# Kernel tuning notes

Measured on AMD Instinct MI355X. Metric: run time of the kernel, lower is better.

## Reference

```python
import jax, jax.numpy as jnp
import numpy as np

TEMP_DIM = 36      # V
HIDDEN   = 128     # d
HEADS    = 4
STATIC   = 16
MAX_LEN  = 500
SEQ_T    = 256
BATCH    = 32


def _xavier(k, shape):
    lim = np.sqrt(6.0 / (shape[0] + shape[1]))
    return jax.random.uniform(k, shape, jnp.float32, -lim, lim)


def setup_inputs() -> dict:
    d, V, S, T, B = HIDDEN, TEMP_DIM, STATIC, SEQ_T, BATCH
    key = jax.random.key(0)
    ks = jax.random.split(key, 16)
    return dict(
        Xtemp=jax.random.normal(ks[0], (T, B, V), jnp.float32),
        Xtimes=jax.random.uniform(ks[1], (T, B, 1), jnp.float32) * MAX_LEN,
        Xstatic=jax.random.normal(ks[2], (B, S), jnp.float32),
        mask=jax.random.randint(ks[3], (T, B, V), 0, 2, jnp.int32),
        # MultiHeadAttention params
        Wq=_xavier(ks[4], (d, d)), Wk=_xavier(ks[5], (d, d)), Wv=_xavier(ks[6], (d, d)),
        # grouped Conv1d(V, V*d, 1, groups=V): per-variable scale+bias -> (V,d)
        temp_w=jax.random.normal(ks[7], (V, d), jnp.float32) * 0.5,
        temp_b=jnp.zeros((V, d), jnp.float32),
        # static embedding Linear(S, V*d)
        emb_W=_xavier(ks[8], (S, V * d)), emb_b=jnp.zeros((V * d,), jnp.float32),
        # MLP: Conv1d(V*d,4d,1)+BN+GELU, Conv1d(4d,d,1)+BN+GELU
        mlp_W1=_xavier(ks[9], (4 * d, V * d)), mlp_b1=jnp.zeros((4 * d,), jnp.float32),
        bn1_g=jnp.ones((4 * d,), jnp.float32), bn1_b=jnp.zeros((4 * d,), jnp.float32),
        mlp_W2=_xavier(ks[10], (d, 4 * d)), mlp_b2=jnp.zeros((d,), jnp.float32),
        bn2_g=jnp.ones((d,), jnp.float32), bn2_b=jnp.zeros((d,), jnp.float32),
        ln_g=jnp.ones((d,), jnp.float32), ln_b=jnp.zeros((d,), jnp.float32),
    )


def _batchnorm(x, g, b):
    # train-mode BatchNorm1d over (B, T) for x:(B, C, T), biased variance, eps=1e-5
    mu = x.mean((0, 2), keepdims=True)
    var = x.var((0, 2), keepdims=True)
    return (x - mu) * jax.lax.rsqrt(var + 1e-5) * g[None, :, None] + b[None, :, None]


def reference(Xtemp, Xtimes, Xstatic, mask, Wq, Wk, Wv, temp_w, temp_b,
              emb_W, emb_b, mlp_W1, mlp_b1, bn1_g, bn1_b,
              mlp_W2, mlp_b2, bn2_g, bn2_b, ln_g, ln_b):
    T, B, V = Xtemp.shape
    d = Wq.shape[0]
    h = HEADS
    dk = d // h

    xt = Xtemp.transpose(1, 2, 0)                      # (B,V,T)
    m = mask.astype(jnp.float32).transpose(1, 2, 0)    # (B,V,T)

    # grouped 1x1 conv == per-variable affine lift to d channels
    Htemp = xt[:, :, None, :] * temp_w[None, :, :, None] + temp_b[None, :, :, None]  # (B,V,d,T)
    Htemp = Htemp.transpose(0, 2, 1, 3)                # (B,d,V,T)

    # positional encoding
    timescales = jnp.power(jnp.float32(MAX_LEN), jnp.linspace(0.0, 1.0, d // 2))
    scaled = Xtimes / timescales                       # (T,B,d//2)
    pe = jnp.concatenate([jnp.sin(scaled), jnp.cos(scaled)], axis=-1)  # (T,B,d)
    Hpos = pe.transpose(1, 2, 0)[:, :, None, :]        # (B,d,1,T)

    emb = (Xstatic @ emb_W + emb_b).reshape(B, V, d).transpose(0, 2, 1)[..., None]  # (B,d,V,1)
    H = Htemp + Hpos + emb                             # (B,d,V,T)

    # masked temporal mean per variable
    mk = m[:, None]                                    # (B,1,V,T)
    h2 = (H * mk).sum(-1)                              # (B,d,V)
    lt = mk.sum(-1) + 1.0                              # (B,1,V)
    h4 = (h2 / lt).transpose(0, 2, 1)                  # (B,V,d)

    # multi-head variable-vs-variable scores
    scale = 1.0 / np.sqrt(dk).astype(np.float32)
    q = (h4 @ Wq).reshape(B, V, h, dk) * scale
    k = (h4 @ Wk).reshape(B, V, h, dk) * scale
    A = jnp.einsum('bvhd,buhd->bhvu', q, k)            # (B,h,V,V)
    mean_v = h4 @ Wv                                   # (B,V,d)

    # per-timestep key masking, broadcast softmax over last (key-variable) dim
    key_mask = m.transpose(0, 2, 1)                    # (B,T,V)
    A4 = A[:, :, None, :, :] - 1e6 * (1.0 - key_mask[:, None, :, None, :])  # (B,h,T,V,V)
    S = jax.nn.softmax(A4, axis=-1)                    # (B,h,T,V,V)

    H2 = H.reshape(B, h, dk, V, T)
    v2 = jnp.einsum('bhtvu,bhdut->bhdvt', S, H2)       # (B,h,dk,V,T)
    v3 = v2.reshape(B, d, V, T)
    v4 = v3 + mean_v.transpose(0, 2, 1)[:, :, :, None]
    v5 = v4.reshape(B, d * V, T)

    y1 = jnp.einsum('bct,oc->bot', v5, mlp_W1) + mlp_b1[None, :, None]
    y1 = jax.nn.gelu(_batchnorm(y1, bn1_g, bn1_b), approximate=False)
    y2 = jnp.einsum('bct,oc->bot', y1, mlp_W2) + mlp_b2[None, :, None]
    z = jax.nn.gelu(_batchnorm(y2, bn2_g, bn2_b), approximate=False)   # (B,d,T)

    # residual LayerNorm over channel dim
    zt = z.transpose(0, 2, 1)                          # (B,T,d)
    mu = zt.mean(-1, keepdims=True)
    var = zt.var(-1, keepdims=True)
    zn = (zt - mu) * jax.lax.rsqrt(var + 1e-5) * ln_g + ln_b
    return z + zn.transpose(0, 2, 1)                   # (B,d,T)
```

## Files before the change

### kernel.cpp

```cpp
#include <hip/hip_runtime.h>
#include <hip/hip_bf16.h>
#include <math.h>

#define T_  256
#define B_  32
#define V_  36
#define D_  128
#define H_  4
#define DK_ 32
#define S_  16
#define D4_ 512
#define K1_ 4608
#define M_  8192

typedef __hip_bfloat16 bf16;
typedef __attribute__((ext_vector_type(8))) short short8;
typedef __attribute__((ext_vector_type(4))) float f32x4;

__device__ __forceinline__ float gelu_f(float x){
    return 0.5f * x * (1.0f + erff(x * 0.70710678118654752f));
}

__device__ __forceinline__ float dot4(float4 a, float4 b){
    return fmaf(a.x, b.x, fmaf(a.y, b.y, fmaf(a.z, b.z, a.w * b.w)));
}

__device__ __forceinline__ unsigned short bf16_bits(float x){
    bf16 h = __float2bfloat16(x);
    return *reinterpret_cast<unsigned short*>(&h);
}

#define GLD16(g, l) __builtin_amdgcn_global_load_lds( \
    (const __attribute__((address_space(1))) void*)(g), \
    (__attribute__((address_space(3))) void*)(l), 16, 0, 0)

__global__ void k_pe(const float* __restrict__ Xtimes, const float* __restrict__ Xtemp,
                     const int* __restrict__ mask, float* __restrict__ PE,
                     float* __restrict__ QQ){
    int bt = blockIdx.x;
    int b = bt >> 8, t = bt & 255;
    int tid = threadIdx.x;
    float x = Xtimes[t*B_ + b];
    int i = (tid < 64) ? tid : tid - 64;
    float sc = x * exp2f(-(float)i * (8.965784284662087f / 63.0f));
    PE[(size_t)bt*D_ + tid] = (tid < 64) ? sinf(sc) : cosf(sc);
    if(tid < 64){
        float m = 0.f, xv = 0.f;
        if(tid < V_){
            m  = (float)mask[(t*B_ + b)*V_ + tid];
            xv = Xtemp[(t*B_ + b)*V_ + tid];
        }
        float s = m;
        #pragma unroll
        for(int off = 32; off > 0; off >>= 1) s += __shfl_xor(s, off);
        if(tid < V_){
            float q0 = (s > 0.f) ? m : 1.f;
            float q1 = (s > 0.f) ? m*xv : xv;
            QQ[(size_t)bt*80 + tid]      = q1;
            QQ[(size_t)bt*80 + 40 + tid] = q0;
        }
    }
}

__global__ void k_cb(const float* __restrict__ Xstatic, const float* __restrict__ embW,
                     const float* __restrict__ embB, const float* __restrict__ tempB,
                     float* __restrict__ CB, float* __restrict__ cbP){
    int bv = blockIdx.x;
    int b = bv / V_, v = bv - (bv / V_) * V_;
    int dd = threadIdx.x;
    int c = v*D_ + dd;
    float acc = tempB[c] + embB[c];
    #pragma unroll
    for(int s = 0; s < S_; ++s) acc = fmaf(Xstatic[b*S_+s], embW[s*K1_ + c], acc);
    CB[(size_t)bv*D_ + dd] = acc;
    cbP[(((size_t)b*9 + (v >> 2))*D_ + dd)*4 + (v & 3)] = acc;
}

__global__ void k_packtw(const float* __restrict__ tempW, float* __restrict__ twP){
    int v = blockIdx.x, dd = threadIdx.x;
    twP[(((v >> 2))*D_ + dd)*4 + (v & 3)] = tempW[v*D_ + dd];
}

__global__ void k_h4(const float* __restrict__ Xtemp, const int* __restrict__ mask,
                     const float* __restrict__ PE, const float* __restrict__ tempW,
                     const float* __restrict__ CB, float* __restrict__ H4){
    __shared__ float s_m[T_];
    __shared__ float s_r0[256];
    __shared__ float s_r1[256];
    __shared__ float s_p[2][D_];
    int bv = blockIdx.x;
    int b = bv / V_, v = bv - (bv / V_) * V_;
    int tid = threadIdx.x;
    float mval = (float)mask[(tid*B_ + b)*V_ + v];
    float xval = Xtemp[(tid*B_ + b)*V_ + v];
    s_m[tid]  = mval;
    s_r0[tid] = mval;
    s_r1[tid] = mval * xval;
    __syncthreads();
    for(int off = 128; off > 0; off >>= 1){
        if(tid < off){ s_r0[tid] += s_r0[tid+off]; s_r1[tid] += s_r1[tid+off]; }
        __syncthreads();
    }
    float sm = s_r0[0], sx = s_r1[0];
    int dd = tid & 127, half = tid >> 7;
    float sp = 0.f;
    for(int tt = half*128; tt < half*128 + 128; ++tt)
        sp = fmaf(s_m[tt], PE[(size_t)(b*T_ + tt)*D_ + dd], sp);
    s_p[half][dd] = sp;
    __syncthreads();
    if(tid < D_){
        float spv = s_p[0][tid] + s_p[1][tid];
        float h2 = fmaf(sx, tempW[v*D_ + tid], fmaf(sm, CB[(size_t)bv*D_ + tid], spv));
        H4[(size_t)bv*D_ + tid] = h2 / (sm + 1.0f);
    }
}

__global__ void k_qkv(const float* __restrict__ H4, const float* __restrict__ Wq,
                      const float* __restrict__ Wk, const float* __restrict__ Wv,
                      float* __restrict__ QS, float* __restrict__ KS, float* __restrict__ MV){
    __shared__ float s_h[D_];
    int bv = blockIdx.x;
    int o = threadIdx.x;
    s_h[o] = H4[(size_t)bv*D_ + o];
    __syncthreads();
    float aq = 0.f, ak = 0.f, av = 0.f;
    #pragma unroll 8
    for(int kk = 0; kk < D_; ++kk){
        float hv = s_h[kk];
        aq = fmaf(hv, Wq[kk*D_ + o], aq);
        ak = fmaf(hv, Wk[kk*D_ + o], ak);
        av = fmaf(hv, Wv[kk*D_ + o], av);
    }
    const float scale = 0.17677669529663687f;
    QS[(size_t)bv*D_ + o] = aq * scale;
    KS[(size_t)bv*D_ + o] = ak * scale;
    MV[(size_t)bv*D_ + o] = av;
}

__global__ void k_attE(const float* __restrict__ QS, const float* __restrict__ KS,
                       float* __restrict__ E){
    int id = blockIdx.x;
    int v  = id % V_;
    int bh = id / V_;
    int hh = bh & 3, b = bh >> 2;
    int u = threadIdx.x;
    __shared__ float s_q[DK_];
    if(u < DK_) s_q[u] = QS[(size_t)(b*V_ + v)*D_ + hh*DK_ + u];
    __syncthreads();
    float a = -INFINITY;
    if(u < V_){
        a = 0.f;
        const float* kp = &KS[(size_t)(b*V_ + u)*D_ + hh*DK_];
        #pragma unroll
        for(int kk = 0; kk < DK_; ++kk) a = fmaf(s_q[kk], kp[kk], a);
    }
    float m = a;
    for(int off = 32; off > 0; off >>= 1) m = fmaxf(m, __shfl_xor(m, off));
    if(u < V_) E[(size_t)id*40 + u] = expf(a - m);
}

__global__ __launch_bounds__(256) void k_v5(const float* __restrict__ QQ,
        const float* __restrict__ Eg, const float* __restrict__ twP,
        const float* __restrict__ cbP, const float* __restrict__ MV,
        const float* __restrict__ PE, bf16* __restrict__ V5){
    __shared__ float s_E[4*1300];
    int bt = blockIdx.x;
    int b = bt >> 8;
    int tid = threadIdx.x;
    int vq = tid >> 6, hh = (tid >> 4) & 3, j = tid & 15;
    int dd0 = hh*32 + j, dd1 = dd0 + 16;

    for(int i = tid; i < 144*9; i += 256){
        int hv = i / 9, u4 = i - hv*9;
        int hq = hv / 36, vr = hv - hq*36;
        float4 e = *(const float4*)&Eg[((size_t)b*144 + hv)*40 + u4*4];
        *(float4*)&s_E[hq*1300 + (u4*36 + vr)*4] = e;
    }
    __syncthreads();

    float acc0[9] = {}, acc1[9] = {}, den[9] = {};
    const float* qq = &QQ[(size_t)bt*80];
    #pragma unroll 1
    for(int u4 = 0; u4 < 9; ++u4){
        float4 q1 = *(const float4*)&qq[u4*4];
        float4 q0 = *(const float4*)&qq[40 + u4*4];
        float4 tw0 = *(const float4*)&twP[(u4*D_ + dd0)*4];
        float4 tw1 = *(const float4*)&twP[(u4*D_ + dd1)*4];
        float4 cb0 = *(const float4*)&cbP[(((size_t)b*9 + u4)*D_ + dd0)*4];
        float4 cb1 = *(const float4*)&cbP[(((size_t)b*9 + u4)*D_ + dd1)*4];
        float4 w0, w1;
        w0.x = fmaf(q1.x, tw0.x, q0.x*cb0.x); w0.y = fmaf(q1.y, tw0.y, q0.y*cb0.y);
        w0.z = fmaf(q1.z, tw0.z, q0.z*cb0.z); w0.w = fmaf(q1.w, tw0.w, q0.w*cb0.w);
        w1.x = fmaf(q1.x, tw1.x, q0.x*cb1.x); w1.y = fmaf(q1.y, tw1.y, q0.y*cb1.y);
        w1.z = fmaf(q1.z, tw1.z, q0.z*cb1.z); w1.w = fmaf(q1.w, tw1.w, q0.w*cb1.w);
        const float* eb = &s_E[hh*1300 + (u4*36 + vq*9)*4];
        #pragma unroll
        for(int vv = 0; vv < 9; ++vv){
            float4 e = *(const float4*)&eb[vv*4];
            den[vv]  += dot4(e, q0);
            acc0[vv] += dot4(e, w0);
            acc1[vv] += dot4(e, w1);
        }
    }
    float pe0 = PE[(size_t)bt*D_ + dd0];
    float pe1 = PE[(size_t)bt*D_ + dd1];
    bf16* op0 = V5 + (size_t)bt*K1_ + dd0*V_ + vq*9;
    bf16* op1 = V5 + (size_t)bt*K1_ + dd1*V_ + vq*9;
    #pragma unroll
    for(int vv = 0; vv < 9; ++vv){
        float rd = 1.0f / den[vv];
        float m0v = MV[((size_t)b*V_ + vq*9 + vv)*D_ + dd0];
        float m1v = MV[((size_t)b*V_ + vq*9 + vv)*D_ + dd1];
        op0[vv] = __float2bfloat16(fmaf(acc0[vv], rd, m0v + pe0));
        op1[vv] = __float2bfloat16(fmaf(acc1[vv], rd, m1v + pe1));
    }
}

__global__ void k_cast(const float* __restrict__ src, bf16* __restrict__ dst){
    int i = (blockIdx.x*256 + threadIdx.x)*4;
    float4 v = *(const float4*)&src[i];
    dst[i+0] = __float2bfloat16(v.x);
    dst[i+1] = __float2bfloat16(v.y);
    dst[i+2] = __float2bfloat16(v.z);
    dst[i+3] = __float2bfloat16(v.w);
}

__global__ __launch_bounds__(256) void k_gemm1(const bf16* __restrict__ A,
        const bf16* __restrict__ Bw, const float* __restrict__ bias,
        float* __restrict__ C){
    __shared__ __align__(16) bf16 As[128*64];
    __shared__ __align__(16) bf16 Bs[64*64];
    int bid = blockIdx.x;
    int L = (bid & 7)*64 + (bid >> 3);
    int nb = L & 7, mb = L >> 3;
    int m0 = mb * 128, n0 = nb * 64;
    int tid = threadIdx.x;
    int w = tid >> 6, l = tid & 63;
    int wr = w >> 1, wc = w & 1;
    int r = l & 15, kg = l >> 4;
    f32x4 acc[4][2] = {};

    int sA0 = 0*256 + w*64 + l;
    int sA1 = 1*256 + w*64 + l;
    int sA2 = 2*256 + w*64 + l;
    int sA3 = 3*256 + w*64 + l;
    int sB0 = 0*256 + w*64 + l;
    int sB1 = 1*256 + w*64 + l;
    const bf16* gA0 = A + (size_t)(m0 + (sA0>>3))*K1_ + ((sA0&7) ^ ((sA0>>3)&7))*8;
    const bf16* gA1 = A + (size_t)(m0 + (sA1>>3))*K1_ + ((sA1&7) ^ ((sA1>>3)&7))*8;
    const bf16* gA2 = A + (size_t)(m0 + (sA2>>3))*K1_ + ((sA2&7) ^ ((sA2>>3)&7))*8;
    const bf16* gA3 = A + (size_t)(m0 + (sA3>>3))*K1_ + ((sA3&7) ^ ((sA3>>3)&7))*8;
    const bf16* gB0 = Bw + (size_t)(n0 + (sB0>>3))*K1_ + ((sB0&7) ^ ((sB0>>3)&7))*8;
    const bf16* gB1 = Bw + (size_t)(n0 + (sB1>>3))*K1_ + ((sB1&7) ^ ((sB1>>3)&7))*8;
    bf16* lA0 = &As[(0*256 + w*64)*8];
    bf16* lA1 = &As[(1*256 + w*64)*8];
    bf16* lA2 = &As[(2*256 + w*64)*8];
    bf16* lA3 = &As[(3*256 + w*64)*8];
    bf16* lB0 = &Bs[(0*256 + w*64)*8];
    bf16* lB1 = &Bs[(1*256 + w*64)*8];

    for(int k0 = 0; k0 < K1_; k0 += 64){
        GLD16(gA0 + k0, lA0);
        GLD16(gA1 + k0, lA1);
        GLD16(gA2 + k0, lA2);
        GLD16(gA3 + k0, lA3);
        GLD16(gB0 + k0, lB0);
        GLD16(gB1 + k0, lB1);
        __syncthreads();
        short8 af[2][4], bfr[2][2];
        #pragma unroll
        for(int kh = 0; kh < 2; ++kh){
            #pragma unroll
            for(int m = 0; m < 4; ++m){
                int row = wr*64 + m*16 + r;
                int e = (row*64 + kh*32 + kg*8) ^ ((r & 7) << 3);
                af[kh][m] = *(const short8*)&As[e];
            }
            #pragma unroll
            for(int n = 0; n < 2; ++n){
                int row = wc*32 + n*16 + r;
                int e = (row*64 + kh*32 + kg*8) ^ ((r & 7) << 3);
                bfr[kh][n] = *(const short8*)&Bs[e];
            }
        }
        #pragma unroll
        for(int kh = 0; kh < 2; ++kh)
            #pragma unroll
            for(int m = 0; m < 4; ++m)
                #pragma unroll
                for(int n = 0; n < 2; ++n)
                    acc[m][n] = __builtin_amdgcn_mfma_f32_16x16x32_bf16(
                                    af[kh][m], bfr[kh][n], acc[m][n], 0, 0, 0);
        __syncthreads();
    }
    #pragma unroll
    for(int m = 0; m < 4; ++m){
        int rowb = m0 + wr*64 + m*16 + kg*4;
        #pragma unroll
        for(int n = 0; n < 2; ++n){
            int col = n0 + wc*32 + n*16 + r;
            float bv = bias[col];
            #pragma unroll
            for(int i = 0; i < 4; ++i)
                C[(size_t)(rowb + i)*D4_ + col] = acc[m][n][i] + bv;
        }
    }
}

__global__ void k_stats(const float* __restrict__ X, int C, float* __restrict__ ST){
    int r0 = blockIdx.x * 32;
    int tid = threadIdx.x;
    for(int c = tid; c < C; c += 256){
        float s = 0.f, q = 0.f;
        for(int r = 0; r < 32; ++r){
            float v = X[(size_t)(r0 + r)*C + c];
            s += v;
            q = fmaf(v, v, q);
        }
        atomicAdd(&ST[c], s);
        atomicAdd(&ST[C + c], q);
    }
}

__global__ void k_bnfin(const float* __restrict__ ST, const float* __restrict__ g,
                        const float* __restrict__ bb, int C, float* __restrict__ P){
    int c = blockIdx.x * blockDim.x + threadIdx.x;
    if(c < C){
        float mu  = ST[c] * (1.0f / M_);
        float var = ST[C + c] * (1.0f / M_) - mu*mu;
        float sc  = g[c] * rsqrtf(var + 1e-5f);
        P[c]     = sc;
        P[C + c] = bb[c] - mu*sc;
    }
}

__global__ __launch_bounds__(256) void k_gemm2(const float* __restrict__ Y1,
        const float* __restrict__ P1, const bf16* __restrict__ W2b,
        const float* __restrict__ b2, float* __restrict__ Z){
    __shared__ __align__(16) bf16 As[64*64];
    __shared__ __align__(16) bf16 Bs[64*64];
    int m0 = blockIdx.x * 64, n0 = blockIdx.y * 64;
    int tid = threadIdx.x;
    int w = tid >> 6, l = tid & 63;
    int wr = w >> 1, wc = w & 1;
    int r = l & 15, kg = l >> 4;
    f32x4 acc[2][2] = {};

    int sB0 = 0*256 + w*64 + l;
    int sB1 = 1*256 + w*64 + l;
    const bf16* gB0 = W2b + (size_t)(n0 + (sB0>>3))*D4_ + ((sB0&7) ^ ((sB0>>3)&7))*8;
    const bf16* gB1 = W2b + (size_t)(n0 + (sB1>>3))*D4_ + ((sB1&7) ^ ((sB1>>3)&7))*8;
    bf16* lB0 = &Bs[(0*256 + w*64)*8];
    bf16* lB1 = &Bs[(1*256 + w*64)*8];

    int arow = tid >> 2;
    int akq  = (tid & 3) * 16;
    int k8a  = (tid & 3) * 2;
    int e0 = arow*64 + ((k8a+0) ^ (arow & 7))*8;
    int e1 = arow*64 + ((k8a+1) ^ (arow & 7))*8;

    for(int k0 = 0; k0 < D4_; k0 += 64){
        GLD16(gB0 + k0, lB0);
        GLD16(gB1 + k0, lB1);
        const float* ya = &Y1[(size_t)(m0 + arow)*D4_ + k0 + akq];
        const float* sc = &P1[k0 + akq];
        const float* sh = &P1[D4_ + k0 + akq];
        unsigned int pk[8];
        #pragma unroll
        for(int q = 0; q < 4; ++q){
            float4 y  = *(const float4*)&ya[q*4];
            float4 s4 = *(const float4*)&sc[q*4];
            float4 h4 = *(const float4*)&sh[q*4];
            float a0 = gelu_f(fmaf(y.x, s4.x, h4.x));
            float a1 = gelu_f(fmaf(y.y, s4.y, h4.y));
            float a2 = gelu_f(fmaf(y.z, s4.z, h4.z));
            float a3 = gelu_f(fmaf(y.w, s4.w, h4.w));
            pk[q*2+0] = (unsigned)bf16_bits(a0) | ((unsigned)bf16_bits(a1) << 16);
            pk[q*2+1] = (unsigned)bf16_bits(a2) | ((unsigned)bf16_bits(a3) << 16);
        }
        uint4 wA0 = {pk[0], pk[1], pk[2], pk[3]};
        uint4 wA1 = {pk[4], pk[5], pk[6], pk[7]};
        *(uint4*)&As[e0] = wA0;
        *(uint4*)&As[e1] = wA1;
        __syncthreads();
        short8 af[2][2], bfr[2][2];
        #pragma unroll
        for(int kh = 0; kh < 2; ++kh){
            #pragma unroll
            for(int m = 0; m < 2; ++m){
                int row = wr*32 + m*16 + r;
                int e = (row*64 + kh*32 + kg*8) ^ ((r & 7) << 3);
                af[kh][m] = *(const short8*)&As[e];
            }
            #pragma unroll
            for(int n = 0; n < 2; ++n){
                int row = wc*32 + n*16 + r;
                int e = (row*64 + kh*32 + kg*8) ^ ((r & 7) << 3);
                bfr[kh][n] = *(const short8*)&Bs[e];
            }
        }
        #pragma unroll
        for(int kh = 0; kh < 2; ++kh)
            #pragma unroll
            for(int m = 0; m < 2; ++m)
                #pragma unroll
                for(int n = 0; n < 2; ++n)
                    acc[m][n] = __builtin_amdgcn_mfma_f32_16x16x32_bf16(
                                    af[kh][m], bfr[kh][n], acc[m][n], 0, 0, 0);
        __syncthreads();
    }
    #pragma unroll
    for(int m = 0; m < 2; ++m){
        int rowb = m0 + wr*32 + m*16 + kg*4;
        #pragma unroll
        for(int n = 0; n < 2; ++n){
            int col = n0 + wc*32 + n*16 + r;
            float bv = b2[col];
            #pragma unroll
            for(int i = 0; i < 4; ++i)
                Z[(size_t)(rowb + i)*D_ + col] = acc[m][n][i] + bv;
        }
    }
}

__global__ __launch_bounds__(256) void k_final(const float* __restrict__ Z,
        const float* __restrict__ P2, const float* __restrict__ lng,
        const float* __restrict__ lnb, float* __restrict__ out){
    __shared__ float s_z[64*129];
    __shared__ float s_mu[64];
    __shared__ float s_rs[64];
    int b  = blockIdx.x >> 2;
    int t0 = (blockIdx.x & 3) * 64;
    int tid = threadIdx.x;
    #pragma unroll
    for(int i = 0; i < 32; ++i){
        int idx = tid + i*256;
        int row = idx >> 7, col = idx & 127;
        float v = Z[(size_t)(b*T_ + t0 + row)*D_ + col];
        s_z[row*129 + col] = gelu_f(fmaf(v, P2[col], P2[D_ + col]));
    }
    __syncthreads();
    if(tid < 64){
        float s = 0.f;
        #pragma unroll
        for(int j = 0; j < D_; ++j) s += s_z[tid*129 + j];
        float mu = s * (1.0f / D_);
        float q = 0.f;
        #pragma unroll
        for(int j = 0; j < D_; ++j){
            float dv = s_z[tid*129 + j] - mu;
            q = fmaf(dv, dv, q);
        }
        s_mu[tid] = mu;
        s_rs[tid] = rsqrtf(q * (1.0f / D_) + 1e-5f);
    }
    __syncthreads();
    int o  = tid & 127;
    int th = tid >> 7;
    float g  = lng[o];
    float be = lnb[o];
    #pragma unroll
    for(int j4 = 0; j4 < 8; ++j4){
        float4 ov;
        #pragma unroll
        for(int q = 0; q < 4; ++q){
            int tt = th*32 + j4*4 + q;
            float z = s_z[tt*129 + o];
            float zn = fmaf((z - s_mu[tt]) * s_rs[tt], g, be);
            (&ov.x)[q] = z + zn;
        }
        *(float4*)&out[((size_t)(b*D_ + o))*T_ + t0 + th*32 + j4*4] = ov;
    }
}

extern "C" void kernel_launch(void* const* d_in, const int* in_sizes, int n_in,
                              void* d_out, int out_size, void* d_ws, size_t ws_size,
                              hipStream_t stream){
    const float* Xtemp   = (const float*)d_in[0];
    const float* Xtimes  = (const float*)d_in[1];
    const float* Xstatic = (const float*)d_in[2];
    const int*   mask    = (const int*)  d_in[3];
    const float* Wq      = (const float*)d_in[4];
    const float* Wk      = (const float*)d_in[5];
    const float* Wv      = (const float*)d_in[6];
    const float* tempW   = (const float*)d_in[7];
    const float* tempB   = (const float*)d_in[8];
    const float* embW    = (const float*)d_in[9];
    const float* embB    = (const float*)d_in[10];
    const float* W1      = (const float*)d_in[11];
    const float* b1      = (const float*)d_in[12];
    const float* bn1g    = (const float*)d_in[13];
    const float* bn1b    = (const float*)d_in[14];
    const float* W2      = (const float*)d_in[15];
    const float* b2      = (const float*)d_in[16];
    const float* bn2g    = (const float*)d_in[17];
    const float* bn2b    = (const float*)d_in[18];
    const float* lng     = (const float*)d_in[19];
    const float* lnb     = (const float*)d_in[20];
    float* out = (float*)d_out;

    float* w = (float*)d_ws;
    float* PE = w;  w += (size_t)M_ * D_;
    float* CB = w;  w += (size_t)B_ * V_ * D_;
    float* cbP= w;  w += (size_t)B_ * 9 * D_ * 4;
    float* twP= w;  w += (size_t)9 * D_ * 4;
    float* H4 = w;  w += (size_t)B_ * V_ * D_;
    float* QS = w;  w += (size_t)B_ * V_ * D_;
    float* KS = w;  w += (size_t)B_ * V_ * D_;
    float* MV = w;  w += (size_t)B_ * V_ * D_;
    float* E  = w;  w += (size_t)B_ * 144 * 40;
    float* QQ = w;  w += (size_t)M_ * 80;
    float* Y1 = w;  w += (size_t)M_ * D4_;
    float* Z1 = w;  w += (size_t)M_ * D_;
    float* ST1 = w; w += 1024;
    float* ST2 = w; w += 256;
    float* P1  = w; w += 1024;
    float* P2  = w; w += 256;
    bf16* V5  = (bf16*)w;
    bf16* W1b = V5 + (size_t)M_ * K1_;
    bf16* W2b = W1b + (size_t)D4_ * K1_;

    hipMemsetAsync(ST1, 0, (1024 + 256) * sizeof(float), stream);

    k_pe    <<<M_, D_, 0, stream>>>(Xtimes, Xtemp, mask, PE, QQ);
    k_cb    <<<B_*V_, D_, 0, stream>>>(Xstatic, embW, embB, tempB, CB, cbP);
    k_packtw<<<V_, D_, 0, stream>>>(tempW, twP);
    k_cast  <<<(D4_*K1_)/1024, 256, 0, stream>>>(W1, W1b);
    k_cast  <<<(D_*D4_)/1024, 256, 0, stream>>>(W2, W2b);
    k_h4    <<<B_*V_, 256, 0, stream>>>(Xtemp, mask, PE, tempW, CB, H4);
    k_qkv   <<<B_*V_, D_, 0, stream>>>(H4, Wq, Wk, Wv, QS, KS, MV);
    k_attE  <<<B_*H_*V_, 64, 0, stream>>>(QS, KS, E);
    k_v5    <<<M_, 256, 0, stream>>>(QQ, E, twP, cbP, MV, PE, V5);
    k_gemm1 <<<512, 256, 0, stream>>>(V5, W1b, b1, Y1);
    k_stats <<<M_/32, 256, 0, stream>>>(Y1, D4_, ST1);
    k_bnfin <<<2, 256, 0, stream>>>(ST1, bn1g, bn1b, D4_, P1);
    k_gemm2 <<<dim3(M_/64, D_/64), 256, 0, stream>>>(Y1, P1, W2b, b2, Z1);
    k_stats <<<M_/32, 256, 0, stream>>>(Z1, D_, ST2);
    k_bnfin <<<1, 128, 0, stream>>>(ST2, bn2g, bn2b, D_, P2);
    k_final <<<B_*(T_/64), 256, 0, stream>>>(Z1, P2, lng, lnb, out);
}
```

Before: 390.3 us.

## Batch 8 timesteps per k_v5 block, split denominator kernel, permute V5 layout

k_v5 now processes 8 timesteps per block, so the per-batch E tile is staged into shared memory once per 8 timesteps instead of once per timestep. The softmax denominator moves to a separate k_den kernel that writes reciprocals to a new workspace buffer. The V5 output layout changes from dd-major to v-major, so stores become contiguous across threads, and W1 is cast with a matching column permutation so the GEMM result is unchanged. The costs are an extra kernel launch, an extra global buffer round trip for the reciprocals, and fewer, more serial blocks in k_v5.

```diff
diff --git a/kernel.cpp b/kernel.cpp
--- a/kernel.cpp
+++ b/kernel.cpp
@@ -159,13 +159,31 @@
     if(u < V_) E[(size_t)id*40 + u] = expf(a - m);
 }
 
+__global__ void k_den(const float* __restrict__ Eg, const float* __restrict__ QQ,
+                      float* __restrict__ RDEN){
+    int bt = blockIdx.x;
+    int b = bt >> 8;
+    int hv = threadIdx.x;
+    if(hv < 144){
+        const float* q0 = &QQ[(size_t)bt*80 + 40];
+        const float* ep = &Eg[((size_t)b*144 + hv)*40];
+        float den = 0.f;
+        #pragma unroll
+        for(int u4 = 0; u4 < 9; ++u4)
+            den += dot4(*(const float4*)&ep[u4*4], *(const float4*)&q0[u4*4]);
+        RDEN[(size_t)bt*144 + hv] = 1.0f / den;
+    }
+}
+
 __global__ __launch_bounds__(256) void k_v5(const float* __restrict__ QQ,
         const float* __restrict__ Eg, const float* __restrict__ twP,
         const float* __restrict__ cbP, const float* __restrict__ MV,
-        const float* __restrict__ PE, bf16* __restrict__ V5){
+        const float* __restrict__ PE, const float* __restrict__ RDEN,
+        bf16* __restrict__ V5){
     __shared__ float s_E[4*1300];
-    int bt = blockIdx.x;
-    int b = bt >> 8;
+    int blk = blockIdx.x;
+    int b = blk >> 5, tgrp = blk & 31;
+    int bt0 = b*T_ + tgrp*8;
     int tid = threadIdx.x;
     int vq = tid >> 6, hh = (tid >> 4) & 3, j = tid & 15;
     int dd0 = hh*32 + j, dd1 = dd0 + 16;
@@ -178,42 +196,52 @@
     }
     __syncthreads();
 
-    float acc0[9] = {}, acc1[9] = {}, den[9] = {};
-    const float* qq = &QQ[(size_t)bt*80];
     #pragma unroll 1
-    for(int u4 = 0; u4 < 9; ++u4){
-        float4 q1 = *(const float4*)&qq[u4*4];
-        float4 q0 = *(const float4*)&qq[40 + u4*4];
-        float4 tw0 = *(const float4*)&twP[(u4*D_ + dd0)*4];
-        float4 tw1 = *(const float4*)&twP[(u4*D_ + dd1)*4];
-        float4 cb0 = *(const float4*)&cbP[(((size_t)b*9 + u4)*D_ + dd0)*4];
-        float4 cb1 = *(const float4*)&cbP[(((size_t)b*9 + u4)*D_ + dd1)*4];
-        float4 w0, w1;
-        w0.x = fmaf(q1.x, tw0.x, q0.x*cb0.x); w0.y = fmaf(q1.y, tw0.y, q0.y*cb0.y);
-        w0.z = fmaf(q1.z, tw0.z, q0.z*cb0.z); w0.w = fmaf(q1.w, tw0.w, q0.w*cb0.w);
-        w1.x = fmaf(q1.x, tw1.x, q0.x*cb1.x); w1.y = fmaf(q1.y, tw1.y, q0.y*cb1.y);
-        w1.z = fmaf(q1.z, tw1.z, q0.z*cb1.z); w1.w = fmaf(q1.w, tw1.w, q0.w*cb1.w);
-        const float* eb = &s_E[hh*1300 + (u4*36 + vq*9)*4];
+    for(int tg = 0; tg < 8; ++tg){
+        int bt = bt0 + tg;
+        const float* qq = &QQ[(size_t)bt*80];
+        float acc0[9] = {}, acc1[9] = {};
+        #pragma unroll 1
+        for(int u4 = 0; u4 < 9; ++u4){
+            float4 q1 = *(const float4*)&qq[u4*4];
+            float4 q0 = *(const float4*)&qq[40 + u4*4];
+            float4 tw0 = *(const float4*)&twP[(u4*D_ + dd0)*4];
+            float4 tw1 = *(const float4*)&twP[(u4*D_ + dd1)*4];
+            float4 cb0 = *(const float4*)&cbP[(((size_t)b*9 + u4)*D_ + dd0)*4];
+            float4 cb1 = *(const float4*)&cbP[(((size_t)b*9 + u4)*D_ + dd1)*4];
+            float4 w0, w1;
+            w0.x = fmaf(q1.x, tw0.x, q0.x*cb0.x); w0.y = fmaf(q1.y, tw0.y, q0.y*cb0.y);
+            w0.z = fmaf(q1.z, tw0.z, q0.z*cb0.z); w0.w = fmaf(q1.w, tw0.w, q0.w*cb0.w);
+            w1.x = fmaf(q1.x, tw1.x, q0.x*cb1.x); w1.y = fmaf(q1.y, tw1.y, q0.y*cb1.y);
+            w1.z = fmaf(q1.z, tw1.z, q0.z*cb1.z); w1.w = fmaf(q1.w, tw1.w, q0.w*cb1.w);
+            const float* eb = &s_E[hh*1300 + (u4*36 + vq*9)*4];
+            #pragma unroll
+            for(int vv = 0; vv < 9; ++vv){
+                float4 e = *(const float4*)&eb[vv*4];
+                acc0[vv] += dot4(e, w0);
+                acc1[vv] += dot4(e, w1);
+            }
+        }
+        float pe0 = PE[(size_t)bt*D_ + dd0];
+        float pe1 = PE[(size_t)bt*D_ + dd1];
+        const float* rdp = &RDEN[(size_t)bt*144 + hh*36 + vq*9];
+        bf16* op = V5 + (size_t)bt*K1_;
         #pragma unroll
         for(int vv = 0; vv < 9; ++vv){
-            float4 e = *(const float4*)&eb[vv*4];
-            den[vv]  += dot4(e, q0);
-            acc0[vv] += dot4(e, w0);
-            acc1[vv] += dot4(e, w1);
-        }
-    }
-    float pe0 = PE[(size_t)bt*D_ + dd0];
-    float pe1 = PE[(size_t)bt*D_ + dd1];
-    bf16* op0 = V5 + (size_t)bt*K1_ + dd0*V_ + vq*9;
-    bf16* op1 = V5 + (size_t)bt*K1_ + dd1*V_ + vq*9;
-    #pragma unroll
-    for(int vv = 0; vv < 9; ++vv){
-        float rd = 1.0f / den[vv];
-        float m0v = MV[((size_t)b*V_ + vq*9 + vv)*D_ + dd0];
-        float m1v = MV[((size_t)b*V_ + vq*9 + vv)*D_ + dd1];
-        op0[vv] = __float2bfloat16(fmaf(acc0[vv], rd, m0v + pe0));
-        op1[vv] = __float2bfloat16(fmaf(acc1[vv], rd, m1v + pe1));
-    }
+            float rd = rdp[vv];
+            float m0v = MV[((size_t)b*V_ + vq*9 + vv)*D_ + dd0];
+            float m1v = MV[((size_t)b*V_ + vq*9 + vv)*D_ + dd1];
+            op[(vq*9 + vv)*D_ + dd0] = __float2bfloat16(fmaf(acc0[vv], rd, m0v + pe0));
+            op[(vq*9 + vv)*D_ + dd1] = __float2bfloat16(fmaf(acc1[vv], rd, m1v + pe1));
+        }
+    }
+}
+
+__global__ void k_castw1(const float* __restrict__ src, bf16* __restrict__ dst){
+    int i = blockIdx.x*256 + threadIdx.x;
+    int o = i / K1_, c = i - o*K1_;
+    int v = c >> 7, dd = c & 127;
+    dst[i] = __float2bfloat16(src[(size_t)o*K1_ + dd*V_ + v]);
 }
 
 __global__ void k_cast(const float* __restrict__ src, bf16* __restrict__ dst){
@@ -510,6 +538,7 @@
     float* MV = w;  w += (size_t)B_ * V_ * D_;
     float* E  = w;  w += (size_t)B_ * 144 * 40;
     float* QQ = w;  w += (size_t)M_ * 80;
+    float* RD = w;  w += (size_t)M_ * 144;
     float* Y1 = w;  w += (size_t)M_ * D4_;
     float* Z1 = w;  w += (size_t)M_ * D_;
     float* ST1 = w; w += 1024;
@@ -525,12 +554,13 @@
     k_pe    <<<M_, D_, 0, stream>>>(Xtimes, Xtemp, mask, PE, QQ);
     k_cb    <<<B_*V_, D_, 0, stream>>>(Xstatic, embW, embB, tempB, CB, cbP);
     k_packtw<<<V_, D_, 0, stream>>>(tempW, twP);
-    k_cast  <<<(D4_*K1_)/1024, 256, 0, stream>>>(W1, W1b);
+    k_castw1<<<(D4_*K1_)/256, 256, 0, stream>>>(W1, W1b);
     k_cast  <<<(D_*D4_)/1024, 256, 0, stream>>>(W2, W2b);
     k_h4    <<<B_*V_, 256, 0, stream>>>(Xtemp, mask, PE, tempW, CB, H4);
     k_qkv   <<<B_*V_, D_, 0, stream>>>(H4, Wq, Wk, Wv, QS, KS, MV);
     k_attE  <<<B_*H_*V_, 64, 0, stream>>>(QS, KS, E);
-    k_v5    <<<M_, 256, 0, stream>>>(QQ, E, twP, cbP, MV, PE, V5);
+    k_den   <<<M_, 192, 0, stream>>>(E, QQ, RD);
+    k_v5    <<<B_*(T_/8), 256, 0, stream>>>(QQ, E, twP, cbP, MV, PE, RD, V5);
     k_gemm1 <<<512, 256, 0, stream>>>(V5, W1b, b1, Y1);
     k_stats <<<M_/32, 256, 0, stream>>>(Y1, D4_, ST1);
     k_bnfin <<<2, 256, 0, stream>>>(ST1, bn1g, bn1b, D4_, P1);
```

After: 382.0 us. -2.1%, faster.
